# Performance work log

Hardware: AMD Instinct MI355X
Metric: run time of the kernel (lower is better)

## Reference

```python
import jax, jax.numpy as jnp
import numpy as np

# 8-bit signed quantizer bounds and integer-rescale constant (from module attrs)
X1_LO, X1_HI = -128.0, 127.0
X2_LO, X2_HI = -128.0, 127.0
Y_LO, Y_HI = -128.0, 127.0
G_VALUE = 16.0


def setup_inputs() -> dict:
    key = jax.random.key(0)
    k1, k2 = jax.random.split(key)
    # Pre-quantized integer activations stored as float32 (as in int-infer mode)
    x1 = jnp.round(jnp.clip(jax.random.normal(k1, (2, 16, 2048, 64), dtype=jnp.float32) * 40.0, X1_LO, X1_HI))
    x2 = jnp.round(jnp.clip(jax.random.normal(k2, (2, 16, 64, 2048), dtype=jnp.float32) * 40.0, X2_LO, X2_HI))
    return {
        "x1": x1,
        "x2": x2,
        "scale1_last_layer": jnp.float32(0.1),
        "scale_x1": jnp.float32(0.05),
        "scale2_last_layer": jnp.float32(0.08),
        "scale_x2": jnp.float32(0.04),
    }


def _div_shift(x, scale_prev, scale_cur, lo, hi):
    # round(x * s_prev / s_cur) then clamp to quantizer bounds
    return jnp.clip(jnp.round(x * (scale_prev / scale_cur)), lo, hi)


def reference(x1, x2, scale1_last_layer, scale_x1, scale2_last_layer, scale_x2):
    # _forward_infer: rescale both operands, integer matmul, /G, round, clip
    x1_int = _div_shift(x1, scale1_last_layer, scale_x1, X1_LO, X1_HI)
    x2_int = _div_shift(x2, scale2_last_layer, scale_x2, X2_LO, X2_HI)
    # [b, h, s, d] @ [b, h, d, s] -> [b, h, s, s]
    y_int = jnp.clip(jnp.round(jnp.matmul(x1_int, x2_int) / G_VALUE), Y_LO, Y_HI)
    return y_int
```

## Files before the change

kernel.cpp:

```cpp
#include <hip/hip_runtime.h>


typedef int   v4i  __attribute__((ext_vector_type(4)));
typedef int   v16i __attribute__((ext_vector_type(16)));
typedef float v4f  __attribute__((ext_vector_type(4)));

static constexpr int BATCH = 32;
static constexpr int SEQ   = 2048;
static constexpr int DIM   = 64;
static constexpr int TILE  = 128;
static constexpr int TPB   = 256;
static constexpr int TPS   = SEQ / TILE;
static constexpr int TPBATCH = TPS * TPS;
static constexpr int NBLK  = BATCH * TPBATCH;
static constexpr size_t PKB = (size_t)BATCH * SEQ * DIM;

__device__ __forceinline__ int qpack4(v4f v, float r) {
    int dw = 0;
    #pragma unroll
    for (int j = 0; j < 4; ++j) {
        float q = rintf(v[j] * r);
        q = fminf(fmaxf(q, -128.f), 127.f);
        dw |= ((int)q & 0xFF) << (8 * j);
    }
    return dw;
}

__global__ __launch_bounds__(256) void prepack_b_kernel(
    const float* __restrict__ x2,
    const float* __restrict__ p_s2ll, const float* __restrict__ p_sx2,
    char* __restrict__ B8)
{
    const float r2 = p_s2ll[0] / p_sx2[0];
    const int t  = (int)blockIdx.x * 256 + (int)threadIdx.x;
    const int b  = t >> 13;
    const int kq = (t >> 11) & 3;
    const int n  = t & 2047;
    const float* src = x2 + (size_t)b * DIM * SEQ + (size_t)(kq * 16) * SEQ + n;
    v4i pk;
    #pragma unroll
    for (int d = 0; d < 4; ++d) {
        int dw = 0;
        #pragma unroll
        for (int j = 0; j < 4; ++j) {
            float q = rintf(src[(size_t)(4 * d + j) * SEQ] * r2);
            q = fminf(fmaxf(q, -128.f), 127.f);
            dw |= ((int)q & 0xFF) << (8 * j);
        }
        pk[d] = dw;
    }
    *(v4i*)(B8 + (size_t)t * 16) = pk;
}

__global__ __launch_bounds__(TPB) void oint_mm_packed(
    const float* __restrict__ x1,
    const float* __restrict__ p_s1ll, const float* __restrict__ p_sx1,
    const char* __restrict__ B8,
    float* __restrict__ out)
{
    __shared__ float slab[TPB / 64][32 * 64];

    const float r1 = p_s1ll[0] / p_sx1[0];

    const int bid     = (int)blockIdx.x;
    const int logical = (bid & 7) * (NBLK >> 3) + (bid >> 3);

    const int batch = logical >> 8;
    const int t     = logical & (TPBATCH - 1);
    const int tm    = t >> 4;
    const int tn    = t & (TPS - 1);

    const float* Abase = x1 + (size_t)batch * SEQ * DIM;
    float*       Obase = out + (size_t)batch * SEQ * SEQ;

    const int tid  = (int)threadIdx.x;
    const int lane = tid & 63;
    const int wave = tid >> 6;
    const int wr   = wave >> 1;
    const int wc   = wave & 1;

    const int mbase = tm * TILE + wr * 64;
    const int nbase = tn * TILE + wc * 64;

    const int lc = lane & 31;
    const int kh = lane >> 5;

    float* ws = slab[wave];

    v4i bfrag[2][2];
    #pragma unroll
    for (int fn = 0; fn < 2; ++fn)
        #pragma unroll
        for (int s = 0; s < 2; ++s)
            bfrag[fn][s] = *(const v4i*)(
                B8 + ((size_t)(batch * 4 + s * 2 + kh) * SEQ + nbase + fn * 32 + lc) * 16);

    #pragma unroll
    for (int fm = 0; fm < 2; ++fm) {
        v4i af[2];
        #pragma unroll
        for (int s = 0; s < 2; ++s) {
            const float* src = Abase + (size_t)(mbase + fm * 32 + lc) * DIM + s * 32 + kh * 16;
            v4i pk;
            #pragma unroll
            for (int d = 0; d < 4; ++d) pk[d] = qpack4(*(const v4f*)(src + 4 * d), r1);
            af[s] = pk;
        }

        #pragma unroll
        for (int fn = 0; fn < 2; ++fn) {
            v16i z = {0,0,0,0,0,0,0,0,0,0,0,0,0,0,0,0};
            v16i acc = __builtin_amdgcn_mfma_i32_32x32x32_i8(af[0], bfrag[fn][0], z,   0, 0, 0);
            acc      = __builtin_amdgcn_mfma_i32_32x32x32_i8(af[1], bfrag[fn][1], acc, 0, 0, 0);

            #pragma unroll
            for (int r = 0; r < 16; ++r) {
                const int rloc = (r & 3) + 8 * (r >> 2) + 4 * kh;
                float v = rintf((float)acc[r] * 0.0625f);
                v = fminf(fmaxf(v, -128.f), 127.f);
                ws[rloc * 64 + fn * 32 + lc] = v;
            }
        }

        #pragma unroll
        for (int i = 0; i < 8; ++i) {
            const int f = i * 64 + lane;
            const int r = f >> 4;
            const int q = f & 15;
            v4f v = *(const v4f*)&ws[r * 64 + q * 4];
            const int grow = mbase + fm * 32 + r;
            __builtin_nontemporal_store(
                v, (v4f*)(Obase + (size_t)grow * SEQ + nbase + q * 4));
        }
    }
}

extern "C" void kernel_launch(void* const* d_in, const int* in_sizes, int n_in,
                              void* d_out, int out_size, void* d_ws, size_t ws_size,
                              hipStream_t stream) {
    (void)in_sizes; (void)n_in; (void)out_size; (void)ws_size;
    const float* x1 = (const float*)d_in[0];
    const float* x2 = (const float*)d_in[1];
    const float* s1 = (const float*)d_in[2];
    const float* s2 = (const float*)d_in[3];
    const float* s3 = (const float*)d_in[4];
    const float* s4 = (const float*)d_in[5];
    float* out = (float*)d_out;

    char* B8 = (char*)d_ws;
    prepack_b_kernel<<<1024, 256, 0, stream>>>(x2, s3, s4, B8);
    oint_mm_packed<<<NBLK, TPB, 0, stream>>>(x1, s1, s2, B8, out);
}
```

Measured before the change: 100.6 us.

## Reshape output tile to 64x256 with shared staging for full-row coalesced stores

Changes each block's output tile from 128x128 to 64x256, with all four waves sharing one LDS staging buffer. Each wave now covers a 64-column strip, and the whole block writes 1 KB contiguous row segments instead of per-wave 256 B segments. The aim is to make the nontemporal output stores, which dominate this write-bound kernel, more contiguous. In exchange it adds block-wide __syncthreads barriers and gives up per-wave independence, and A-quantization work per block is unchanged while B reuse differs.

```diff
diff --git a/kernel.cpp b/kernel.cpp
--- a/kernel.cpp
+++ b/kernel.cpp
@@ -8,10 +8,12 @@
 static constexpr int BATCH = 32;
 static constexpr int SEQ   = 2048;
 static constexpr int DIM   = 64;
-static constexpr int TILE  = 128;
+static constexpr int TM    = 64;
+static constexpr int TN    = 256;
 static constexpr int TPB   = 256;
-static constexpr int TPS   = SEQ / TILE;
-static constexpr int TPBATCH = TPS * TPS;
+static constexpr int TPSM  = SEQ / TM;
+static constexpr int TPSN  = SEQ / TN;
+static constexpr int TPBATCH = TPSM * TPSN;
 static constexpr int NBLK  = BATCH * TPBATCH;
 static constexpr size_t PKB = (size_t)BATCH * SEQ * DIM;
 
@@ -58,7 +60,7 @@
     const char* __restrict__ B8,
     float* __restrict__ out)
 {
-    __shared__ float slab[TPB / 64][32 * 64];
+    __shared__ float slab[32 * 256];
 
     const float r1 = p_s1ll[0] / p_sx1[0];
 
@@ -67,8 +69,8 @@
 
     const int batch = logical >> 8;
     const int t     = logical & (TPBATCH - 1);
-    const int tm    = t >> 4;
-    const int tn    = t & (TPS - 1);
+    const int tm    = t >> 3;
+    const int tn    = t & (TPSN - 1);
 
     const float* Abase = x1 + (size_t)batch * SEQ * DIM;
     float*       Obase = out + (size_t)batch * SEQ * SEQ;
@@ -76,16 +78,12 @@
     const int tid  = (int)threadIdx.x;
     const int lane = tid & 63;
     const int wave = tid >> 6;
-    const int wr   = wave >> 1;
-    const int wc   = wave & 1;
 
-    const int mbase = tm * TILE + wr * 64;
-    const int nbase = tn * TILE + wc * 64;
+    const int mbase = tm * TM;
+    const int nbase = tn * TN + wave * 64;
 
     const int lc = lane & 31;
     const int kh = lane >> 5;
-
-    float* ws = slab[wave];
 
     v4i bfrag[2][2];
     #pragma unroll
@@ -97,6 +95,8 @@
 
     #pragma unroll
     for (int fm = 0; fm < 2; ++fm) {
+        if (fm) __syncthreads();
+
         v4i af[2];
         #pragma unroll
         for (int s = 0; s < 2; ++s) {
@@ -116,21 +116,24 @@
             #pragma unroll
             for (int r = 0; r < 16; ++r) {
                 const int rloc = (r & 3) + 8 * (r >> 2) + 4 * kh;
+                const int c    = wave * 64 + fn * 32 + lc;
                 float v = rintf((float)acc[r] * 0.0625f);
                 v = fminf(fmaxf(v, -128.f), 127.f);
-                ws[rloc * 64 + fn * 32 + lc] = v;
+                slab[rloc * 256 + c] = v;
             }
         }
 
+        __syncthreads();
+
         #pragma unroll
         for (int i = 0; i < 8; ++i) {
-            const int f = i * 64 + lane;
-            const int r = f >> 4;
-            const int q = f & 15;
-            v4f v = *(const v4f*)&ws[r * 64 + q * 4];
+            const int f = i * TPB + tid;
+            const int r = f >> 6;
+            const int q = f & 63;
+            v4f v = *(const v4f*)&slab[r * 256 + q * 4];
             const int grow = mbase + fm * 32 + r;
             __builtin_nontemporal_store(
-                v, (v4f*)(Obase + (size_t)grow * SEQ + nbase + q * 4));
+                v, (v4f*)(Obase + (size_t)grow * SEQ + tn * TN + q * 4));
         }
     }
 }
```

After: 96.33 us. 4.3% less time.
